# Kernel optimization log

Measured on AMD Instinct MI355X. Metric: run time of the kernel, lower is better.

The kernel has to match this reference:

```python
import jax, jax.numpy as jnp
import numpy as np

N_NODES = 100000
N_EDGES = 600000
IN_FEAT = 128
OUT_FEAT = 128
NUM_RELS = 8
NUM_BASES = 4


def setup_inputs() -> dict:
    key = jax.random.key(0)
    ks = jax.random.split(key, 8)
    h = jax.random.normal(ks[0], (N_NODES, IN_FEAT), dtype=jnp.float32)
    # xavier-ish scale for params
    weight = jax.random.normal(ks[1], (NUM_BASES, IN_FEAT, OUT_FEAT), dtype=jnp.float32) * (1.0 / np.sqrt(IN_FEAT))
    w_comp = jax.random.normal(ks[2], (NUM_RELS, NUM_BASES), dtype=jnp.float32) * (1.0 / np.sqrt(NUM_BASES))
    root_weight = jax.random.normal(ks[3], (IN_FEAT, OUT_FEAT), dtype=jnp.float32) * (1.0 / np.sqrt(IN_FEAT))
    bias = jnp.zeros((OUT_FEAT,), dtype=jnp.float32)
    src = jax.random.randint(ks[4], (N_EDGES,), 0, N_NODES, dtype=jnp.int32)
    dst = jax.random.randint(ks[5], (N_EDGES,), 0, N_NODES, dtype=jnp.int32)
    rel_type = jax.random.randint(ks[6], (N_EDGES,), 0, NUM_RELS, dtype=jnp.int32)
    return {"h": h, "weight": weight, "w_comp": w_comp, "root_weight": root_weight,
            "bias": bias, "src": src, "dst": dst, "rel_type": rel_type}


def reference(h, weight, w_comp, root_weight, bias, src, dst, rel_type):
    # Basis decomposition: W[r] = sum_b w_comp[r,b] * weight[b]
    B, I, O = weight.shape
    R = w_comp.shape[0]
    W = (w_comp @ weight.reshape(B, I * O)).reshape(R, I, O)  # [R, in, out]
    # msg_e = h[src_e] @ W[rel_e]; computed as all-relation projection + gather
    # (avoids materializing [E, in, out] per-edge weights)
    proj = jnp.einsum('ni,rio->nro', h, W)          # [N, R, out]
    msg = proj[src, rel_type]                        # [E, out]
    agg = jax.ops.segment_sum(msg, dst, num_segments=h.shape[0])  # scatter-sum
    out = h @ root_weight + agg + bias
    return jax.nn.relu(out)
```

## Files before the change

### kernel.cpp

```cpp
#include <hip/hip_runtime.h>
#include <hip/hip_bf16.h>

#define N_NODES 100000
#define N_EDGES 600000
#define FEAT 128
#define NUM_RELS 8
#define NUM_BASES 4
#define NBE 2344

#define PREP_CAST 6250
#define PREP_BLDB 320
#define PREP_ZERO 392
#define PREP_GRID (PREP_CAST + PREP_BLDB + PREP_ZERO)

#define SCAN_TILES 98

typedef short bf16x8 __attribute__((ext_vector_type(8)));
typedef float f32x4  __attribute__((ext_vector_type(4)));
typedef float f32x2  __attribute__((ext_vector_type(2)));

__device__ inline short f2bf(float x) {
    __hip_bfloat16 b = __float2bfloat16(x);
    return *reinterpret_cast<short*>(&b);
}


__global__ __launch_bounds__(256) void k_prep(const float* __restrict__ h,
                                              const float* __restrict__ weight,
                                              const float* __restrict__ rw,
                                              short* __restrict__ hb,
                                              short* __restrict__ Btf,
                                              int* __restrict__ cnt,
                                              int* __restrict__ status) {
    int b = blockIdx.x;
    if (b < PREP_CAST) {
        int i = b * 256 + threadIdx.x;
        const float4* h4 = (const float4*)h;
        float4 v0 = h4[2 * i], v1 = h4[2 * i + 1];
        union { short s[8]; bf16x8 v; } u;
        u.s[0] = f2bf(v0.x); u.s[1] = f2bf(v0.y); u.s[2] = f2bf(v0.z); u.s[3] = f2bf(v0.w);
        u.s[4] = f2bf(v1.x); u.s[5] = f2bf(v1.y); u.s[6] = f2bf(v1.z); u.s[7] = f2bf(v1.w);
        ((bf16x8*)hb)[i] = u.v;
    } else if (b < PREP_CAST + PREP_BLDB) {
        int idx = (b - PREP_CAST) * 256 + threadIdx.x;
        int kc = idx >> 14;
        int e  = idx & 16383;
        int o  = e >> 7, ip = e & 127;
        float v = (kc == 0) ? rw[ip * FEAT + o]
                            : weight[(kc - 1) * FEAT * FEAT + ip * FEAT + o];
        int nt = o & 7, n16 = o >> 3;
        int ks = ip >> 5, quad = (ip >> 3) & 3, j = ip & 7;
        int lane = quad * 16 + n16;
        Btf[((kc * 4 + ks) * 8 + nt) * 512 + lane * 8 + j] = f2bf(v);
    } else {
        int i = (b - PREP_CAST - PREP_BLDB) * 256 + threadIdx.x;
        if (i < N_NODES) cnt[i] = 0;
        else if (i - N_NODES < 128) status[i - N_NODES] = 0;
    }
}

__global__ __launch_bounds__(256) void k_hist_dst(const int* __restrict__ dst,
                                                  int* __restrict__ cnt) {
    int i = blockIdx.x * 256 + threadIdx.x;
    if (i < N_EDGES) atomicAdd(&cnt[dst[i]], 1);
}

__global__ __launch_bounds__(256) void k_scan_lb(const int* __restrict__ cnt,
                                                 int* __restrict__ offs,
                                                 int* __restrict__ cursor,
                                                 int* __restrict__ status) {
    __shared__ int wsum[4];
    __shared__ int bcast;
    int bid = blockIdx.x;
    int lane = threadIdx.x & 63, wid = threadIdx.x >> 6;
    const int N4 = N_NODES / 4;
    int i4 = bid * 256 + threadIdx.x;

    const int4* cnt4 = (const int4*)cnt;
    int4 v = (i4 < N4) ? cnt4[i4] : make_int4(0, 0, 0, 0);
    int s = v.x + v.y + v.z + v.w;
    int incl = s;
#pragma unroll
    for (int d = 1; d < 64; d <<= 1) {
        int t = __shfl_up(incl, d);
        if (lane >= d) incl += t;
    }
    if (lane == 63) wsum[wid] = incl;
    __syncthreads();
    int total = wsum[0] + wsum[1] + wsum[2] + wsum[3];

    if (threadIdx.x < 64) {
        int excl = 0;
        if (bid > 0) {
            if (lane == 0)
                __hip_atomic_store(&status[bid], (total << 2) | 1,
                                   __ATOMIC_RELEASE, __HIP_MEMORY_SCOPE_AGENT);
            int winEnd = bid;
            for (;;) {
                int idx = winEnd - 64 + lane;
                int st = 2;
                if (idx >= 0) {
                    st = __hip_atomic_load(&status[idx],
                                           __ATOMIC_ACQUIRE, __HIP_MEMORY_SCOPE_AGENT);
                    while ((st & 3) == 0) {
                        __builtin_amdgcn_s_sleep(1);
                        st = __hip_atomic_load(&status[idx],
                                               __ATOMIC_ACQUIRE, __HIP_MEMORY_SCOPE_AGENT);
                    }
                }
                unsigned long long done = __ballot((st & 3) == 2);
                int contrib;
                if (done) {
                    int L = 63 - __builtin_clzll(done);
                    contrib = (lane >= L) ? (st >> 2) : 0;
                } else {
                    contrib = st >> 2;
                }
#pragma unroll
                for (int m = 1; m < 64; m <<= 1) contrib += __shfl_xor(contrib, m);
                excl += contrib;
                if (done) break;
                winEnd -= 64;
            }
        }
        if (lane == 0) {
            __hip_atomic_store(&status[bid], ((excl + total) << 2) | 2,
                               __ATOMIC_RELEASE, __HIP_MEMORY_SCOPE_AGENT);
            bcast = excl;
            if (bid == SCAN_TILES - 1) offs[N_NODES] = excl + total;
        }
    }
    __syncthreads();
    int wexcl = 0;
#pragma unroll
    for (int w = 0; w < 4; ++w) if (w < wid) wexcl += wsum[w];
    int base = bcast + wexcl + incl - s;
    if (i4 < N4) {
        int4 ex;
        ex.x = base;
        ex.y = base + v.x;
        ex.z = base + v.x + v.y;
        ex.w = base + v.x + v.y + v.z;
        ((int4*)offs)[i4]   = ex;
        ((int4*)cursor)[i4] = ex;
    }
}

__global__ __launch_bounds__(256) void k_scatter_sorted(const int* __restrict__ src,
                                                        const int* __restrict__ dst,
                                                        const int* __restrict__ rel,
                                                        int* __restrict__ cursor,
                                                        int* __restrict__ packed) {
    int e = blockIdx.x * 256 + threadIdx.x;
    if (e < N_EDGES) {
        int p = atomicAdd(&cursor[dst[e]], 1);
        packed[p] = (src[e] << 3) | rel[e];
    }
}

#define RL(pk, j) __builtin_amdgcn_readlane(pk, j)
#define EDGE_ACC(zz, c, v)                                               \
    {   f32x2 hh; hh.x = __int_as_float((v) << 16);                      \
        hh.y = __int_as_float((v) & 0xffff0000u);                        \
        f32x2 cc;                                                        \
        cc = c.x; zz[0] += cc * hh;                                      \
        cc = c.y; zz[1] += cc * hh;                                      \
        cc = c.z; zz[2] += cc * hh;                                      \
        cc = c.w; zz[3] += cc * hh; }

__global__ __launch_bounds__(256) void k_edge_z(const int* __restrict__ offs,
                                                const int* __restrict__ packed,
                                                const float* __restrict__ wc,
                                                const short* __restrict__ hb,
                                                unsigned int* __restrict__ z_u32) {
    int wid = threadIdx.x >> 6, lane = threadIdx.x & 63;
    int d0 = blockIdx.x * 8 + wid * 2;
    int s0 = offs[d0], sM = offs[d0 + 1], e1 = offs[d0 + 2];

    const float4* wc4 = (const float4*)wc;
    const unsigned int* hbu = (const unsigned int*)hb;

    f32x2 za[4] = {(f32x2)0.f, (f32x2)0.f, (f32x2)0.f, (f32x2)0.f};
    f32x2 zb[4] = {(f32x2)0.f, (f32x2)0.f, (f32x2)0.f, (f32x2)0.f};

    int baseA = s0, baseB = sM;
    while (baseA < sM || baseB < e1) {
        int mA = sM - baseA; mA = mA < 0 ? 0 : (mA > 64 ? 64 : mA);
        int mB = e1 - baseB; mB = mB < 0 ? 0 : (mB > 64 ? 64 : mB);
        int pkA = (lane < mA) ? packed[baseA + lane] : 0;
        int pkB = (lane < mB) ? packed[baseB + lane] : 0;
        int jA = 0, jB = 0;

        while (jA + 3 < mA && jB + 3 < mB) {
            int a0 = RL(pkA, jA), a1 = RL(pkA, jA + 1), a2 = RL(pkA, jA + 2), a3 = RL(pkA, jA + 3);
            int b0 = RL(pkB, jB), b1 = RL(pkB, jB + 1), b2 = RL(pkB, jB + 2), b3 = RL(pkB, jB + 3);
            unsigned int va0 = hbu[(size_t)(a0 >> 3) * 64 + lane];
            unsigned int va1 = hbu[(size_t)(a1 >> 3) * 64 + lane];
            unsigned int va2 = hbu[(size_t)(a2 >> 3) * 64 + lane];
            unsigned int va3 = hbu[(size_t)(a3 >> 3) * 64 + lane];
            unsigned int vb0 = hbu[(size_t)(b0 >> 3) * 64 + lane];
            unsigned int vb1 = hbu[(size_t)(b1 >> 3) * 64 + lane];
            unsigned int vb2 = hbu[(size_t)(b2 >> 3) * 64 + lane];
            unsigned int vb3 = hbu[(size_t)(b3 >> 3) * 64 + lane];
            float4 ca0 = wc4[a0 & 7], ca1 = wc4[a1 & 7], ca2 = wc4[a2 & 7], ca3 = wc4[a3 & 7];
            float4 cb0 = wc4[b0 & 7], cb1 = wc4[b1 & 7], cb2 = wc4[b2 & 7], cb3 = wc4[b3 & 7];
            EDGE_ACC(za, ca0, va0); EDGE_ACC(za, ca1, va1);
            EDGE_ACC(za, ca2, va2); EDGE_ACC(za, ca3, va3);
            EDGE_ACC(zb, cb0, vb0); EDGE_ACC(zb, cb1, vb1);
            EDGE_ACC(zb, cb2, vb2); EDGE_ACC(zb, cb3, vb3);
            jA += 4; jB += 4;
        }
        while (jA < mA && jB < mB) {
            int a0 = RL(pkA, jA), b0 = RL(pkB, jB);
            unsigned int va0 = hbu[(size_t)(a0 >> 3) * 64 + lane];
            unsigned int vb0 = hbu[(size_t)(b0 >> 3) * 64 + lane];
            float4 ca0 = wc4[a0 & 7], cb0 = wc4[b0 & 7];
            EDGE_ACC(za, ca0, va0);
            EDGE_ACC(zb, cb0, vb0);
            ++jA; ++jB;
        }
        while (jA + 3 < mA) {
            int a0 = RL(pkA, jA), a1 = RL(pkA, jA + 1), a2 = RL(pkA, jA + 2), a3 = RL(pkA, jA + 3);
            unsigned int va0 = hbu[(size_t)(a0 >> 3) * 64 + lane];
            unsigned int va1 = hbu[(size_t)(a1 >> 3) * 64 + lane];
            unsigned int va2 = hbu[(size_t)(a2 >> 3) * 64 + lane];
            unsigned int va3 = hbu[(size_t)(a3 >> 3) * 64 + lane];
            float4 ca0 = wc4[a0 & 7], ca1 = wc4[a1 & 7], ca2 = wc4[a2 & 7], ca3 = wc4[a3 & 7];
            EDGE_ACC(za, ca0, va0); EDGE_ACC(za, ca1, va1);
            EDGE_ACC(za, ca2, va2); EDGE_ACC(za, ca3, va3);
            jA += 4;
        }
        while (jA < mA) {
            int a0 = RL(pkA, jA);
            unsigned int va0 = hbu[(size_t)(a0 >> 3) * 64 + lane];
            float4 ca0 = wc4[a0 & 7];
            EDGE_ACC(za, ca0, va0);
            ++jA;
        }
        while (jB + 3 < mB) {
            int b0 = RL(pkB, jB), b1 = RL(pkB, jB + 1), b2 = RL(pkB, jB + 2), b3 = RL(pkB, jB + 3);
            unsigned int vb0 = hbu[(size_t)(b0 >> 3) * 64 + lane];
            unsigned int vb1 = hbu[(size_t)(b1 >> 3) * 64 + lane];
            unsigned int vb2 = hbu[(size_t)(b2 >> 3) * 64 + lane];
            unsigned int vb3 = hbu[(size_t)(b3 >> 3) * 64 + lane];
            float4 cb0 = wc4[b0 & 7], cb1 = wc4[b1 & 7], cb2 = wc4[b2 & 7], cb3 = wc4[b3 & 7];
            EDGE_ACC(zb, cb0, vb0); EDGE_ACC(zb, cb1, vb1);
            EDGE_ACC(zb, cb2, vb2); EDGE_ACC(zb, cb3, vb3);
            jB += 4;
        }
        while (jB < mB) {
            int b0 = RL(pkB, jB);
            unsigned int vb0 = hbu[(size_t)(b0 >> 3) * 64 + lane];
            float4 cb0 = wc4[b0 & 7];
            EDGE_ACC(zb, cb0, vb0);
            ++jB;
        }
        baseA += 64; baseB += 64;
    }

    unsigned int* row0 = z_u32 + (size_t)d0 * 256;
    unsigned int* row1 = row0 + 256;
#pragma unroll
    for (int b = 0; b < 4; ++b) {
        unsigned int lo0 = ((unsigned int)(unsigned short)f2bf(za[b].x));
        unsigned int hi0 = ((unsigned int)(unsigned short)f2bf(za[b].y)) << 16;
        row0[b * 64 + lane] = lo0 | hi0;
        unsigned int lo1 = ((unsigned int)(unsigned short)f2bf(zb[b].x));
        unsigned int hi1 = ((unsigned int)(unsigned short)f2bf(zb[b].y)) << 16;
        row1[b * 64 + lane] = lo1 | hi1;
    }
}

__global__ __launch_bounds__(256) void k_gemm_fused(const short* __restrict__ hb,
                                                    const short* __restrict__ z,
                                                    const short* __restrict__ Btf,
                                                    const float* __restrict__ bias,
                                                    float* __restrict__ out) {
    __shared__ short lds[FEAT * FEAT];
    int wave = threadIdx.x >> 6, lane = threadIdx.x & 63;
    int quad = lane >> 4, n16 = lane & 15;
    int base = blockIdx.x * 128 + wave * 32;

    int rowA0 = base + n16;        if (rowA0 >= N_NODES) rowA0 = N_NODES - 1;
    int rowA1 = base + 16 + n16;   if (rowA1 >= N_NODES) rowA1 = N_NODES - 1;

    f32x4 acc[2][8];
#pragma unroll
    for (int mt = 0; mt < 2; ++mt)
#pragma unroll
        for (int nt = 0; nt < 8; ++nt) acc[mt][nt] = (f32x4)0.f;

    const bf16x8* bp = (const bf16x8*)lds;
    char* lds_base = (char*)lds;

    bf16x8 a_cur[2][4];
    {
        const bf16x8* a0p = (const bf16x8*)(hb + (size_t)rowA0 * FEAT);
        const bf16x8* a1p = (const bf16x8*)(hb + (size_t)rowA1 * FEAT);
#pragma unroll
        for (int ks = 0; ks < 4; ++ks) {
            a_cur[0][ks] = a0p[ks * 4 + quad];
            a_cur[1][ks] = a1p[ks * 4 + quad];
        }
    }

    for (int kc = 0; kc < 5; ++kc) {
        if (kc) __syncthreads();
        const char* gsrc = (const char*)Btf + kc * 32768;
#pragma unroll
        for (int t = 0; t < 8; ++t) {
            unsigned int off = wave * 8192 + t * 1024;
            __builtin_amdgcn_global_load_lds(
                (const __attribute__((address_space(1))) unsigned int*)(gsrc + off + lane * 16),
                (__attribute__((address_space(3))) unsigned int*)(lds_base + off),
                16, 0, 0);
        }
        __syncthreads();

        bf16x8 a_nxt[2][4];
        if (kc < 4) {
            const bf16x8* a0p = (const bf16x8*)(z + (size_t)rowA0 * 512 + kc * FEAT);
            const bf16x8* a1p = (const bf16x8*)(z + (size_t)rowA1 * 512 + kc * FEAT);
#pragma unroll
            for (int ks = 0; ks < 4; ++ks) {
                a_nxt[0][ks] = a0p[ks * 4 + quad];
                a_nxt[1][ks] = a1p[ks * 4 + quad];
            }
        }

#pragma unroll
        for (int ks = 0; ks < 4; ++ks) {
            const bf16x8* bks = bp + ks * 512 + lane;
#pragma unroll
            for (int nt = 0; nt < 8; ++nt) {
                bf16x8 b = bks[nt * 64];
                acc[0][nt] = __builtin_amdgcn_mfma_f32_16x16x32_bf16(a_cur[0][ks], b, acc[0][nt], 0, 0, 0);
                acc[1][nt] = __builtin_amdgcn_mfma_f32_16x16x32_bf16(a_cur[1][ks], b, acc[1][nt], 0, 0, 0);
            }
        }

        if (kc < 4) {
#pragma unroll
            for (int ks = 0; ks < 4; ++ks) {
                a_cur[0][ks] = a_nxt[0][ks];
                a_cur[1][ks] = a_nxt[1][ks];
            }
        }
    }

    float bv[8];
#pragma unroll
    for (int nt = 0; nt < 8; ++nt) bv[nt] = bias[n16 * 8 + nt];

#pragma unroll
    for (int mt = 0; mt < 2; ++mt)
#pragma unroll
        for (int reg = 0; reg < 4; ++reg) {
            int node = base + mt * 16 + quad * 4 + reg;
            if (node < N_NODES) {
                float4 fa, fb;
                fa.x = fmaxf(acc[mt][0][reg] + bv[0], 0.f);
                fa.y = fmaxf(acc[mt][1][reg] + bv[1], 0.f);
                fa.z = fmaxf(acc[mt][2][reg] + bv[2], 0.f);
                fa.w = fmaxf(acc[mt][3][reg] + bv[3], 0.f);
                fb.x = fmaxf(acc[mt][4][reg] + bv[4], 0.f);
                fb.y = fmaxf(acc[mt][5][reg] + bv[5], 0.f);
                fb.z = fmaxf(acc[mt][6][reg] + bv[6], 0.f);
                fb.w = fmaxf(acc[mt][7][reg] + bv[7], 0.f);
                float* row = out + (size_t)node * FEAT + n16 * 8;
                *(float4*)row       = fa;
                *(float4*)(row + 4) = fb;
            }
        }
}


extern "C" void kernel_launch(void* const* d_in, const int* in_sizes, int n_in,
                              void* d_out, int out_size, void* d_ws, size_t ws_size,
                              hipStream_t stream) {
    const float* h    = (const float*)d_in[0];
    const float* wgt  = (const float*)d_in[1];
    const float* wcmp = (const float*)d_in[2];
    const float* rw   = (const float*)d_in[3];
    const float* bias = (const float*)d_in[4];
    const int*   src  = (const int*)d_in[5];
    const int*   dst  = (const int*)d_in[6];
    const int*   rel  = (const int*)d_in[7];
    float* out = (float*)d_out;

    char* ws = (char*)d_ws;
    short*        hb     = (short*)(ws + 0);
    short*        Btf    = (short*)(ws + 25600000ull);
    short*        z      = (short*)(ws + 25763840ull);
    unsigned int* z_u32  = (unsigned int*)z;
    int*          packed = (int*)(ws + 128163840ull);
    int*          cnt    = (int*)(ws + 130563840ull);
    int*          offs   = (int*)(ws + 130963840ull);
    int*          cursor = (int*)(ws + 131363968ull);
    int*          status = (int*)(ws + 131763968ull);

    hipLaunchKernelGGL(k_prep,     dim3(PREP_GRID), dim3(256), 0, stream,
                       h, wgt, rw, hb, Btf, cnt, status);
    hipLaunchKernelGGL(k_hist_dst, dim3(NBE),  dim3(256), 0, stream, dst, cnt);
    hipLaunchKernelGGL(k_scan_lb,  dim3(SCAN_TILES), dim3(256), 0, stream,
                       cnt, offs, cursor, status);
    hipLaunchKernelGGL(k_scatter_sorted, dim3(NBE), dim3(256), 0, stream,
                       src, dst, rel, cursor, packed);
    hipLaunchKernelGGL(k_edge_z,   dim3(N_NODES / 8), dim3(256), 0, stream,
                       offs, packed, wcmp, hb, z_u32);
    hipLaunchKernelGGL(k_gemm_fused, dim3((N_NODES + 127) / 128), dim3(256), 0, stream,
                       hb, z, Btf, bias, out);
}
```

Baseline: 252.4 us.

## Fuse histogram, scan and scatter into one cooperative kernel with grid syncs

Replaces the three counting-sort kernels (dst histogram, decoupled-lookback scan, scatter) with a single cooperative kernel of 1024 blocks. Each thread keeps its up to three edges' dst and packed src/rel in registers across two grid-wide barriers, so src/dst/rel are read once and two kernel launches are removed. The z stores in the edge kernel also become nontemporal stores. In exchange it depends on cooperative launch residency and pays for grid.sync barriers, and most blocks sit idle during the 98-block scan phase.

```diff
diff --git a/kernel.cpp b/kernel.cpp
--- a/kernel.cpp
+++ b/kernel.cpp
@@ -1,12 +1,14 @@
 #include <hip/hip_runtime.h>
 #include <hip/hip_bf16.h>
+#include <hip/hip_cooperative_groups.h>
+
+namespace cg = cooperative_groups;
 
 #define N_NODES 100000
 #define N_EDGES 600000
 #define FEAT 128
 #define NUM_RELS 8
 #define NUM_BASES 4
-#define NBE 2344
 
 #define PREP_CAST 6250
 #define PREP_BLDB 320
@@ -14,6 +16,8 @@
 #define PREP_GRID (PREP_CAST + PREP_BLDB + PREP_ZERO)
 
 #define SCAN_TILES 98
+#define SORT_BLOCKS 1024
+#define SORT_STRIDE (SORT_BLOCKS * 256)
 
 typedef short bf16x8 __attribute__((ext_vector_type(8)));
 typedef float f32x4  __attribute__((ext_vector_type(4)));
@@ -59,102 +63,126 @@
     }
 }
 
-__global__ __launch_bounds__(256) void k_hist_dst(const int* __restrict__ dst,
-                                                  int* __restrict__ cnt) {
-    int i = blockIdx.x * 256 + threadIdx.x;
-    if (i < N_EDGES) atomicAdd(&cnt[dst[i]], 1);
-}
-
-__global__ __launch_bounds__(256) void k_scan_lb(const int* __restrict__ cnt,
-                                                 int* __restrict__ offs,
-                                                 int* __restrict__ cursor,
-                                                 int* __restrict__ status) {
+__global__ __launch_bounds__(256) void k_sort(const int* __restrict__ src,
+                                              const int* __restrict__ dst,
+                                              const int* __restrict__ rel,
+                                              int* __restrict__ cnt,
+                                              int* __restrict__ offs,
+                                              int* __restrict__ cursor,
+                                              int* __restrict__ status,
+                                              int* __restrict__ packed) {
+    cg::grid_group grid = cg::this_grid();
     __shared__ int wsum[4];
     __shared__ int bcast;
-    int bid = blockIdx.x;
-    int lane = threadIdx.x & 63, wid = threadIdx.x >> 6;
-    const int N4 = N_NODES / 4;
-    int i4 = bid * 256 + threadIdx.x;
-
-    const int4* cnt4 = (const int4*)cnt;
-    int4 v = (i4 < N4) ? cnt4[i4] : make_int4(0, 0, 0, 0);
-    int s = v.x + v.y + v.z + v.w;
-    int incl = s;
-#pragma unroll
-    for (int d = 1; d < 64; d <<= 1) {
-        int t = __shfl_up(incl, d);
-        if (lane >= d) incl += t;
-    }
-    if (lane == 63) wsum[wid] = incl;
-    __syncthreads();
-    int total = wsum[0] + wsum[1] + wsum[2] + wsum[3];
-
-    if (threadIdx.x < 64) {
-        int excl = 0;
-        if (bid > 0) {
-            if (lane == 0)
-                __hip_atomic_store(&status[bid], (total << 2) | 1,
-                                   __ATOMIC_RELEASE, __HIP_MEMORY_SCOPE_AGENT);
-            int winEnd = bid;
-            for (;;) {
-                int idx = winEnd - 64 + lane;
-                int st = 2;
-                if (idx >= 0) {
-                    st = __hip_atomic_load(&status[idx],
-                                           __ATOMIC_ACQUIRE, __HIP_MEMORY_SCOPE_AGENT);
-                    while ((st & 3) == 0) {
-                        __builtin_amdgcn_s_sleep(1);
+
+    int g = blockIdx.x * 256 + threadIdx.x;
+
+    int d0v = 0, d1v = 0, d2v = 0, pk0 = 0, pk1 = 0, pk2 = 0;
+    {
+        int e0 = g;
+        d0v = dst[e0]; pk0 = (src[e0] << 3) | rel[e0];
+        atomicAdd(&cnt[d0v], 1);
+        int e1 = g + SORT_STRIDE;
+        if (e1 < N_EDGES) {
+            d1v = dst[e1]; pk1 = (src[e1] << 3) | rel[e1];
+            atomicAdd(&cnt[d1v], 1);
+        }
+        int e2 = g + 2 * SORT_STRIDE;
+        if (e2 < N_EDGES) {
+            d2v = dst[e2]; pk2 = (src[e2] << 3) | rel[e2];
+            atomicAdd(&cnt[d2v], 1);
+        }
+    }
+    grid.sync();
+
+    if (blockIdx.x < SCAN_TILES) {
+        int bid = blockIdx.x;
+        int lane = threadIdx.x & 63, wid = threadIdx.x >> 6;
+        const int N4 = N_NODES / 4;
+        int i4 = bid * 256 + threadIdx.x;
+
+        const int4* cnt4 = (const int4*)cnt;
+        int4 v = (i4 < N4) ? cnt4[i4] : make_int4(0, 0, 0, 0);
+        int s = v.x + v.y + v.z + v.w;
+        int incl = s;
+#pragma unroll
+        for (int dd = 1; dd < 64; dd <<= 1) {
+            int t = __shfl_up(incl, dd);
+            if (lane >= dd) incl += t;
+        }
+        if (lane == 63) wsum[wid] = incl;
+        __syncthreads();
+        int total = wsum[0] + wsum[1] + wsum[2] + wsum[3];
+
+        if (threadIdx.x < 64) {
+            int excl = 0;
+            if (bid > 0) {
+                if (lane == 0)
+                    __hip_atomic_store(&status[bid], (total << 2) | 1,
+                                       __ATOMIC_RELEASE, __HIP_MEMORY_SCOPE_AGENT);
+                int winEnd = bid;
+                for (;;) {
+                    int idx = winEnd - 64 + lane;
+                    int st = 2;
+                    if (idx >= 0) {
                         st = __hip_atomic_load(&status[idx],
                                                __ATOMIC_ACQUIRE, __HIP_MEMORY_SCOPE_AGENT);
+                        while ((st & 3) == 0) {
+                            __builtin_amdgcn_s_sleep(1);
+                            st = __hip_atomic_load(&status[idx],
+                                                   __ATOMIC_ACQUIRE, __HIP_MEMORY_SCOPE_AGENT);
+                        }
                     }
+                    unsigned long long done = __ballot((st & 3) == 2);
+                    int contrib;
+                    if (done) {
+                        int L = 63 - __builtin_clzll(done);
+                        contrib = (lane >= L) ? (st >> 2) : 0;
+                    } else {
+                        contrib = st >> 2;
+                    }
+#pragma unroll
+                    for (int m = 1; m < 64; m <<= 1) contrib += __shfl_xor(contrib, m);
+                    excl += contrib;
+                    if (done) break;
+                    winEnd -= 64;
                 }
-                unsigned long long done = __ballot((st & 3) == 2);
-                int contrib;
-                if (done) {
-                    int L = 63 - __builtin_clzll(done);
-                    contrib = (lane >= L) ? (st >> 2) : 0;
-                } else {
-                    contrib = st >> 2;
-                }
-#pragma unroll
-                for (int m = 1; m < 64; m <<= 1) contrib += __shfl_xor(contrib, m);
-                excl += contrib;
-                if (done) break;
-                winEnd -= 64;
-            }
-        }
-        if (lane == 0) {
-            __hip_atomic_store(&status[bid], ((excl + total) << 2) | 2,
-                               __ATOMIC_RELEASE, __HIP_MEMORY_SCOPE_AGENT);
-            bcast = excl;
-            if (bid == SCAN_TILES - 1) offs[N_NODES] = excl + total;
-        }
-    }
-    __syncthreads();
-    int wexcl = 0;
-#pragma unroll
-    for (int w = 0; w < 4; ++w) if (w < wid) wexcl += wsum[w];
-    int base = bcast + wexcl + incl - s;
-    if (i4 < N4) {
-        int4 ex;
-        ex.x = base;
-        ex.y = base + v.x;
-        ex.z = base + v.x + v.y;
-        ex.w = base + v.x + v.y + v.z;
-        ((int4*)offs)[i4]   = ex;
-        ((int4*)cursor)[i4] = ex;
-    }
-}
-
-__global__ __launch_bounds__(256) void k_scatter_sorted(const int* __restrict__ src,
-                                                        const int* __restrict__ dst,
-                                                        const int* __restrict__ rel,
-                                                        int* __restrict__ cursor,
-                                                        int* __restrict__ packed) {
-    int e = blockIdx.x * 256 + threadIdx.x;
-    if (e < N_EDGES) {
-        int p = atomicAdd(&cursor[dst[e]], 1);
-        packed[p] = (src[e] << 3) | rel[e];
+            }
+            if (lane == 0) {
+                __hip_atomic_store(&status[bid], ((excl + total) << 2) | 2,
+                                   __ATOMIC_RELEASE, __HIP_MEMORY_SCOPE_AGENT);
+                bcast = excl;
+                if (bid == SCAN_TILES - 1) offs[N_NODES] = excl + total;
+            }
+        }
+        __syncthreads();
+        int wexcl = 0;
+#pragma unroll
+        for (int w = 0; w < 4; ++w) if (w < wid) wexcl += wsum[w];
+        int base = bcast + wexcl + incl - s;
+        if (i4 < N4) {
+            int4 ex;
+            ex.x = base;
+            ex.y = base + v.x;
+            ex.z = base + v.x + v.y;
+            ex.w = base + v.x + v.y + v.z;
+            ((int4*)offs)[i4]   = ex;
+            ((int4*)cursor)[i4] = ex;
+        }
+    }
+    grid.sync();
+
+    {
+        int p = atomicAdd(&cursor[d0v], 1);
+        packed[p] = pk0;
+        if (g + SORT_STRIDE < N_EDGES) {
+            int q = atomicAdd(&cursor[d1v], 1);
+            packed[q] = pk1;
+        }
+        if (g + 2 * SORT_STRIDE < N_EDGES) {
+            int r = atomicAdd(&cursor[d2v], 1);
+            packed[r] = pk2;
+        }
     }
 }
 
@@ -264,10 +292,10 @@
     for (int b = 0; b < 4; ++b) {
         unsigned int lo0 = ((unsigned int)(unsigned short)f2bf(za[b].x));
         unsigned int hi0 = ((unsigned int)(unsigned short)f2bf(za[b].y)) << 16;
-        row0[b * 64 + lane] = lo0 | hi0;
+        __builtin_nontemporal_store(lo0 | hi0, &row0[b * 64 + lane]);
         unsigned int lo1 = ((unsigned int)(unsigned short)f2bf(zb[b].x));
         unsigned int hi1 = ((unsigned int)(unsigned short)f2bf(zb[b].y)) << 16;
-        row1[b * 64 + lane] = lo1 | hi1;
+        __builtin_nontemporal_store(lo1 | hi1, &row1[b * 64 + lane]);
     }
 }
 
@@ -399,14 +427,16 @@
     int*          cursor = (int*)(ws + 131363968ull);
     int*          status = (int*)(ws + 131763968ull);
 
-    hipLaunchKernelGGL(k_prep,     dim3(PREP_GRID), dim3(256), 0, stream,
+    hipLaunchKernelGGL(k_prep, dim3(PREP_GRID), dim3(256), 0, stream,
                        h, wgt, rw, hb, Btf, cnt, status);
-    hipLaunchKernelGGL(k_hist_dst, dim3(NBE),  dim3(256), 0, stream, dst, cnt);
-    hipLaunchKernelGGL(k_scan_lb,  dim3(SCAN_TILES), dim3(256), 0, stream,
-                       cnt, offs, cursor, status);
-    hipLaunchKernelGGL(k_scatter_sorted, dim3(NBE), dim3(256), 0, stream,
-                       src, dst, rel, cursor, packed);
-    hipLaunchKernelGGL(k_edge_z,   dim3(N_NODES / 8), dim3(256), 0, stream,
+
+    void* sargs[] = {(void*)&src, (void*)&dst, (void*)&rel,
+                     (void*)&cnt, (void*)&offs, (void*)&cursor,
+                     (void*)&status, (void*)&packed};
+    hipLaunchCooperativeKernel((void*)k_sort, dim3(SORT_BLOCKS), dim3(256),
+                               sargs, 0, stream);
+
+    hipLaunchKernelGGL(k_edge_z, dim3(N_NODES / 8), dim3(256), 0, stream,
                        offs, packed, wcmp, hb, z_u32);
     hipLaunchKernelGGL(k_gemm_fused, dim3((N_NODES + 127) / 128), dim3(256), 0, stream,
                        hb, z, Btf, bias, out);
```

Result: slower. 457.4 us (+81.2%).
